# Performance work log

Measured on AMD Instinct MI355X. Metric: run time of the kernel, lower is better.

## Reference

```python
import jax, jax.numpy as jnp
from jax import lax
import numpy as np

B, M, LH, K, F, NA, NO = 16, 32, 128, 16, 3, 4, 1


def _conv(x, w, b):
    # x: (B,H,W,Cin), w: (kh,kw,Cin,Cout) -> (B,H,W,Cout), SAME zero padding
    return lax.conv_general_dilated(x, w, (1, 1), 'SAME',
                                    dimension_numbers=('NHWC', 'HWIO', 'NHWC')) + b


def setup_inputs() -> dict:
    key = jax.random.key(0)
    ks = jax.random.split(key, 14)
    s = 0.05
    inp = {
        'map_design': jax.random.uniform(ks[0], (B, NO, M, M), jnp.float32),
        'goal_map':   jax.random.uniform(ks[1], (B, 1, M, M), jnp.float32),
        'W_hid': jax.random.normal(ks[2], (3, 3, NO + 1, LH), jnp.float32) * s,
        'b_hid': jax.random.normal(ks[3], (LH,), jnp.float32) * s,
        'W_h0':  jax.random.normal(ks[4], (3, 3, LH, LH), jnp.float32) * s,
        'b_h0':  jax.random.normal(ks[5], (LH,), jnp.float32) * s,
        'W_c0':  jax.random.normal(ks[6], (3, 3, LH, LH), jnp.float32) * s,
        'b_c0':  jax.random.normal(ks[7], (LH,), jnp.float32) * s,
        'W_f':   jax.random.normal(ks[8], (F, F, LH, 1), jnp.float32) * s,
        'b_f':   jax.random.normal(ks[9], (1,), jnp.float32) * s,
        'W_ih':  jax.random.normal(ks[10], (4 * LH, 1), jnp.float32) * s,
        'b_ih':  jax.random.normal(ks[11], (4 * LH,), jnp.float32) * s,
        'W_hh':  jax.random.normal(ks[12], (4 * LH, LH), jnp.float32) * s,
        'b_hh':  jnp.zeros((4 * LH,), jnp.float32),
        'W_pol': jax.random.normal(ks[13], (LH, NA * NO), jnp.float32) * s,
    }
    return inp


def reference(map_design, goal_map, W_hid, b_hid, W_h0, b_h0, W_c0, b_c0,
              W_f, b_f, W_ih, b_ih, W_hh, b_hh, W_pol):
    # NCHW -> NHWC
    X = jnp.concatenate([map_design, goal_map], axis=1).transpose(0, 2, 3, 1)
    hid = _conv(X, W_hid, b_hid)                      # (B,M,M,LH)
    h0 = _conv(hid, W_h0, b_h0)                       # (B,M,M,LH)
    c0 = _conv(hid, W_c0, b_c0)

    def step(carry, _):
        h, c = carry                                  # (B,M,M,LH)
        inp = _conv(h, W_f, b_f).reshape(-1, 1)       # per-pixel scalar input
        hf = h.reshape(-1, LH)
        gates = inp @ W_ih.T + b_ih + hf @ W_hh.T + b_hh   # (BMM, 4*LH)
        i, f, g, o = jnp.split(gates, 4, axis=-1)     # torch LSTMCell order i,f,g,o
        i, f, o = jax.nn.sigmoid(i), jax.nn.sigmoid(f), jax.nn.sigmoid(o)
        g = jnp.tanh(g)
        c2 = f * c.reshape(-1, LH) + i * g
        h2 = o * jnp.tanh(c2)
        return (h2.reshape(B, M, M, LH), c2.reshape(B, M, M, LH)), None

    (hk, _), _ = lax.scan(step, (h0, c0), None, length=K - 1)

    # policy: 1x1 conv == per-pixel matmul
    logits_hw = jnp.einsum('bhwc,ca->bhwa', hk, W_pol)     # (B,M,M,NA*NO)
    logits = logits_hw.transpose(0, 3, 1, 2)               # (B,NA*NO,M,M)
    probs = jax.nn.softmax(logits.reshape(B * NO, NA, M, M), axis=1)
    logits = logits.reshape(B, NO, NA, M, M).transpose(0, 2, 1, 3, 4)
    probs = probs.reshape(B, NO, NA, M, M).transpose(0, 2, 1, 3, 4)
    return logits, probs
```

## Files before the change

kernel.cpp:

```cpp
#include <hip/hip_runtime.h>

#define MM 32
#define LH 128
#define NSTEPS 15
#define SSTR 136
#define NBLK 512
#define FSTR 32
#define SIDX(row,pxi,ch) (((row)*34 + (pxi))*SSTR + (ch))

typedef __bf16  bf16x8  __attribute__((ext_vector_type(8)));
typedef float   floatx4 __attribute__((ext_vector_type(4)));
typedef unsigned long long ull;

#define L2E 1.4426950408889634f

__device__ __forceinline__ float ex2(float x){
#if __has_builtin(__builtin_amdgcn_exp2f)
  return __builtin_amdgcn_exp2f(x);
#else
  float r; asm volatile("v_exp_f32 %0, %1\n\ts_nop 0" : "=v"(r) : "v"(x)); return r;
#endif
}
__device__ __forceinline__ float frcp(float x){ return __builtin_amdgcn_rcpf(x); }

__device__ __forceinline__ unsigned short cvt_bf16(float x){
  __bf16 b = (__bf16)x; unsigned short u; __builtin_memcpy(&u, &b, 2); return u;
}
__device__ __forceinline__ float bf2f(unsigned short u){
  union { unsigned u2; float f; } v; v.u2 = ((unsigned)u) << 16;
  return v.f;
}

__device__ __forceinline__ void st_dev(ull* p, ull v){
  __hip_atomic_store(p, v, __ATOMIC_RELAXED, __HIP_MEMORY_SCOPE_AGENT);
}
__device__ __forceinline__ ull ld_dev(ull* p){
  return __hip_atomic_load(p, __ATOMIC_RELAXED, __HIP_MEMORY_SCOPE_AGENT);
}
__device__ __forceinline__ void wait_flag(int* f, int target){
  while ((int)(__hip_atomic_load(f, __ATOMIC_RELAXED, __HIP_MEMORY_SCOPE_AGENT) - target) < 0){
    __builtin_amdgcn_s_sleep(1);
  }
}
__device__ __forceinline__ void set_flag(int* f, int v){
  __hip_atomic_store(f, v, __ATOMIC_RELAXED, __HIP_MEMORY_SCOPE_AGENT);
}

__global__ __launch_bounds__(512, 4) void k_mega(
    const float* __restrict__ mp,   const float* __restrict__ gl,
    const float* __restrict__ W_hid,const float* __restrict__ b_hid,
    const float* __restrict__ W_h0, const float* __restrict__ b_h0,
    const float* __restrict__ W_c0, const float* __restrict__ b_c0,
    const float* __restrict__ Wf,   const float* __restrict__ bfs,
    const float* __restrict__ wih,  const float* __restrict__ bih,
    const float* __restrict__ Whh,  const float* __restrict__ bhh,
    const float* __restrict__ wpol,
    unsigned short* __restrict__ wc0, unsigned short* __restrict__ wc1,
    unsigned short* __restrict__ whhf, float* __restrict__ bsum,
    unsigned short* __restrict__ wfbF,
    ull* __restrict__ expbuf,
    int* __restrict__ flags, float* __restrict__ out)
{
  __shared__ __attribute__((aligned(16))) unsigned short sH[3*34*SSTR];
  __shared__ float sCv[3][3][36];
  __shared__ float sOwn[32];
  __shared__ float sImp[2][32];

  int t = threadIdx.x, blk = blockIdx.x;
  int y = blk & 31, b = blk >> 5;
  int wave = t >> 6, l = t & 63, m16 = l & 15, quad = l >> 4;
  bool hasU = (y > 0), hasD = (y < 31);
  int ch = wave*16 + m16;

  for (int c = blk*512 + t; c < 91904; c += NBLK*512){
    if (c < 73728){
      int which = (c >= 36864) ? 1 : 0;
      int cc = which ? c - 36864 : c;
      int i2 = cc*4, frag = i2 >> 9, rem = i2 & 511, ll = rem >> 3, e0 = rem & 7;
      int kk = frag >> 5, ct = (frag >> 2) & 7, kc = frag & 3;
      int co = ct*16 + (ll & 15), ci0 = kc*32 + ((ll >> 4) << 3) + e0;
      const float* src = which ? W_c0 : W_h0;
      ull v = 0;
      #pragma unroll
      for (int j=0;j<4;j++) v |= (ull)cvt_bf16(src[(kk<<14) + (ci0+j)*128 + co]) << (16*j);
      st_dev((ull*)(which ? wc1 : wc0) + cc, v);
    } else if (c < 90112){
      int cc = c - 73728;
      int i2 = cc*4, frag = i2 >> 9, rem = i2 & 511, ll = rem >> 3, e0 = rem & 7;
      int q = frag >> 5, ct = (frag >> 2) & 7, kc = frag & 3;
      float scq = (q == 2) ? (2.f*L2E) : (-L2E);
      int rw = q*128 + ct*16 + (ll & 15), col = kc*32 + ((ll >> 4) << 3) + e0;
      const float* s4 = Whh + rw*128 + col;
      ull v = 0;
      #pragma unroll
      for (int j=0;j<4;j++) v |= (ull)cvt_bf16(s4[j]*scq) << (16*j);
      st_dev((ull*)whhf + cc, v);
    } else if (c < 90368){
      int cc = c - 90112; int j = cc*2;
      union { float f[2]; ull u; } pv;
      pv.f[0] = bih[j] + bhh[j]; pv.f[1] = bih[j+1] + bhh[j+1];
      st_dev((ull*)bsum + cc, pv.u);
    } else {
      int cc = c - 90368;
      int i2 = cc*4, frag = i2 >> 9, rem = i2 & 511, ll = rem >> 3, e0 = rem & 7;
      int ky = frag >> 2, kc = frag & 3;
      int n = ll & 15, k0 = kc*32 + ((ll >> 4) << 3) + e0;
      ull v = 0;
      if (n < 3){
        #pragma unroll
        for (int j=0;j<4;j++) v |= (ull)cvt_bf16(Wf[(ky*3 + n)*128 + k0 + j]) << (16*j);
      }
      st_dev((ull*)wfbF + cc, v);
    }
  }
  if (t < 128){
    int p = t >> 6, w2 = t & 63;
    st_dev(expbuf + ((size_t)p*NBLK + blk)*64 + w2, 0);
  }
  __syncthreads();
  if (t == 0) set_flag(&flags[blk*FSTR], 1);

  {
    int hch = t & 127, grp = t >> 7;
    float wz0[9], wz1[9];
    #pragma unroll
    for (int kk=0;kk<9;kk++){ wz0[kk] = W_hid[(kk*2)*LH + hch];
                              wz1[kk] = W_hid[(kk*2+1)*LH + hch]; }
    float bh = b_hid[hch];
    for (int i = 0; i < 24; i++){
      int rp = grp*24 + i, row = rp >> 5, x = rp & 31;
      int yi = y - 1 + row;
      float acc2 = 0.f;
      if (yi >= 0 && yi < MM){
        acc2 = bh;
        #pragma unroll
        for (int ky=0; ky<3; ky++){
          int yy = yi + ky - 1; if (yy < 0 || yy >= MM) continue;
          #pragma unroll
          for (int kx=0; kx<3; kx++){
            int xx = x + kx - 1; if (xx < 0 || xx >= MM) continue;
            int gi = (b*MM + yy)*MM + xx;
            acc2 += mp[gi]*wz0[ky*3+kx] + gl[gi]*wz1[ky*3+kx];
          }
        }
      }
      sH[SIDX(row, x+1, hch)] = cvt_bf16(acc2);
    }
  }
  if (t < 192){
    int k = t >> 6, col = ((t >> 5) & 1) ? 33 : 0, c4 = t & 31;
    *(ull*)&sH[SIDX(k, col, c4*4)] = 0;
  }
  if (t < 3){ sCv[t][0][32] = 0.f; sCv[t][2][1] = 0.f; }
  if (t < 180) wait_flag(&flags[t*FSTR], 1);
  __syncthreads();

  float c_reg[2][4];
  {
    floatx4 acch[2], accc[2];
    #pragma unroll
    for (int mt=0;mt<2;mt++){ acch[mt] = (floatx4){0.f,0.f,0.f,0.f};
                              accc[mt] = (floatx4){0.f,0.f,0.f,0.f}; }
    #pragma unroll
    for (int kk=0; kk<9; kk++){
      int ky = kk/3, kx = kk%3;
      #pragma unroll
      for (int kc=0; kc<4; kc++){
        int frag = ((kk*8 + wave)*4 + kc);
        bf16x8 b0 = *(const bf16x8*)(wc0 + (frag << 9) + l*8);
        bf16x8 b1 = *(const bf16x8*)(wc1 + (frag << 9) + l*8);
        #pragma unroll
        for (int mt=0; mt<2; mt++){
          bf16x8 a = *(const bf16x8*)&sH[SIDX(ky, m16 + mt*16 + kx, kc*32 + quad*8)];
          acch[mt] = __builtin_amdgcn_mfma_f32_16x16x32_bf16(a, b0, acch[mt], 0,0,0);
          accc[mt] = __builtin_amdgcn_mfma_f32_16x16x32_bf16(a, b1, accc[mt], 0,0,0);
        }
      }
    }
    __syncthreads();
    float bh = b_h0[ch], bc = b_c0[ch];
    #pragma unroll
    for (int mt=0; mt<2; mt++)
      #pragma unroll
      for (int r=0; r<4; r++){
        int px = mt*16 + quad*4 + r;
        c_reg[mt][r] = accc[mt][r] + bc;
        sH[SIDX(1, px+1, ch)] = cvt_bf16(acch[mt][r] + bh);
      }
  }
  __syncthreads();

  int cky = (wave == 0) ? 2 : ((wave == 1) ? 0 : 1);
  bf16x8 wfC[4];
  if (wave < 3){
    #pragma unroll
    for (int kc=0;kc<4;kc++)
      wfC[kc] = *(const bf16x8*)(wfbF + (((cky*4 + kc) << 9) + l*8));
  }
  float wv[4], bs[4];
  #pragma unroll
  for (int q=0;q<4;q++){
    float scq = (q == 2) ? (2.f*L2E) : (-L2E);
    int g = q*128 + ch;
    wv[q] = wih[g]*scq; bs[q] = bsum[g]*scq;
  }
  float bf0 = bfs[0];

  for (int s = 0; s < NSTEPS; s++){
    int cur = s & 1;

    bool doRole = (wave == 2) || (wave == 0 && hasU) || (wave == 1 && hasD);
    if (wave < 3 && doRole){
      floatx4 p0 = (floatx4){0.f,0.f,0.f,0.f};
      floatx4 p1 = (floatx4){0.f,0.f,0.f,0.f};
      #pragma unroll
      for (int kc=0;kc<4;kc++){
        bf16x8 aL = *(const bf16x8*)&sH[SIDX(1, m16 + 1,  kc*32 + quad*8)];
        bf16x8 aR = *(const bf16x8*)&sH[SIDX(1, m16 + 17, kc*32 + quad*8)];
        p0 = __builtin_amdgcn_mfma_f32_16x16x32_bf16(aL, wfC[kc], p0, 0,0,0);
        p1 = __builtin_amdgcn_mfma_f32_16x16x32_bf16(aR, wfC[kc], p1, 0,0,0);
      }
      if (m16 < 3){
        #pragma unroll
        for (int r=0;r<4;r++){
          sCv[wave][m16][quad*4 + r + m16]      = p0[r];
          sCv[wave][m16][16 + quad*4 + r + m16] = p1[r];
        }
      }
      __asm__ __volatile__("" ::: "memory");
      if (l < 32){
        float v = sCv[wave][0][l+1] + sCv[wave][1][l+1] + sCv[wave][2][l+1];
        if (wave == 2){
          sOwn[l] = bf0 + v;
        } else {
          union { float f; unsigned u; } pv; pv.f = v;
          st_dev(expbuf + ((size_t)cur*NBLK + blk)*64 + (wave == 1 ? 32 : 0) + l,
                 ((ull)(unsigned)(2 + s) << 32) | (ull)pv.u);
        }
      }
    }

    ull wa = (ull)whhf;
    asm volatile("" : "+v"(wa));
    const unsigned short* wp = (const unsigned short*)wa;
    floatx4 acc[2][4];
    #pragma unroll
    for (int mt=0;mt<2;mt++)
      #pragma unroll
      for (int q=0;q<4;q++) acc[mt][q] = (floatx4){0.f,0.f,0.f,0.f};
    #pragma unroll
    for (int kc=0; kc<4; kc++){
      bf16x8 a0 = *(const bf16x8*)&sH[SIDX(1, m16 + 1,  kc*32 + quad*8)];
      bf16x8 a1 = *(const bf16x8*)&sH[SIDX(1, m16 + 17, kc*32 + quad*8)];
      #pragma unroll
      for (int q=0; q<4; q++){
        bf16x8 bq = *(const bf16x8*)(wp + ((q*32 + wave*4 + kc) << 9) + l*8);
        acc[0][q] = __builtin_amdgcn_mfma_f32_16x16x32_bf16(a0, bq, acc[0][q], 0,0,0);
        acc[1][q] = __builtin_amdgcn_mfma_f32_16x16x32_bf16(a1, bq, acc[1][q], 0,0,0);
      }
    }

    if (wave == 3){
      int d = l >> 5, x = l & 31;
      bool ok = d ? hasD : hasU;
      float v = 0.f;
      if (ok){
        ull* p = expbuf + ((size_t)cur*NBLK + (d ? blk+1 : blk-1))*64 + (d ? 0 : 32) + x;
        ull vv;
        do { vv = ld_dev(p); } while ((int)((unsigned)(vv >> 32) - (unsigned)(2 + s)) < 0);
        union { unsigned u; float f; } pv; pv.u = (unsigned)vv; v = pv.f;
      }
      sImp[d][x] = v;
    }
    __syncthreads();

    #pragma unroll
    for (int mt=0; mt<2; mt++){
      #pragma unroll
      for (int r=0; r<4; r++){
        int px = mt*16 + quad*4 + r;
        float iv = sOwn[px] + sImp[0][px] + sImp[1][px];
        float p0 = acc[mt][0][r] + iv*wv[0] + bs[0];
        float p1 = acc[mt][1][r] + iv*wv[1] + bs[1];
        float p2 = acc[mt][2][r] + iv*wv[2] + bs[2];
        float p3 = acc[mt][3][r] + iv*wv[3] + bs[3];
        float ig = frcp(1.f + ex2(p0));
        float fg = frcp(1.f + ex2(p1));
        float gg = 1.f - 2.f*frcp(1.f + ex2(p2));
        float og = frcp(1.f + ex2(p3));
        float cn = fg*c_reg[mt][r] + ig*gg;
        c_reg[mt][r] = cn;
        float th = 1.f - 2.f*frcp(1.f + ex2((2.f*L2E)*cn));
        sH[SIDX(1, px+1, ch)] = cvt_bf16(og*th);
      }
    }
    __syncthreads();
  }

  {
    int px = t >> 4, s16 = t & 15;
    int base = SIDX(1, px+1, s16*8);
    uint4 h0v = *(const uint4*)&sH[base];
    float la[4] = {0.f,0.f,0.f,0.f};
    const unsigned short* hu = (const unsigned short*)&h0v;
    #pragma unroll
    for (int e=0;e<8;e++){
      int c = s16*8 + e; float hv2 = bf2f(hu[e]);
      const float* w4 = wpol + c*4;
      la[0]+=hv2*w4[0]; la[1]+=hv2*w4[1]; la[2]+=hv2*w4[2]; la[3]+=hv2*w4[3];
    }
    #pragma unroll
    for (int a=0;a<4;a++){
      la[a] += __shfl_xor(la[a], 1, 64);
      la[a] += __shfl_xor(la[a], 2, 64);
      la[a] += __shfl_xor(la[a], 4, 64);
      la[a] += __shfl_xor(la[a], 8, 64);
    }
    if (s16 == 0){
      float m = fmaxf(fmaxf(la[0],la[1]),fmaxf(la[2],la[3]));
      float e[4]; float sum = 0.f;
      #pragma unroll
      for (int a=0;a<4;a++){ e[a]=__expf(la[a]-m); sum+=e[a]; }
      float inv = frcp(sum);
      #pragma unroll
      for (int a=0;a<4;a++){
        int o = ((b*4 + a)*MM + y)*MM + px;
        out[o] = la[a];
        out[65536 + o] = e[a]*inv;
      }
    }
  }
}

extern "C" void kernel_launch(void* const* d_in, const int* in_sizes, int n_in,
                              void* d_out, int out_size, void* d_ws, size_t ws_size,
                              hipStream_t stream){
  const float* mp    = (const float*)d_in[0];
  const float* gl    = (const float*)d_in[1];
  const float* W_hid = (const float*)d_in[2];
  const float* b_hid = (const float*)d_in[3];
  const float* W_h0  = (const float*)d_in[4];
  const float* b_h0  = (const float*)d_in[5];
  const float* W_c0  = (const float*)d_in[6];
  const float* b_c0  = (const float*)d_in[7];
  const float* W_f   = (const float*)d_in[8];
  const float* b_f   = (const float*)d_in[9];
  const float* W_ih  = (const float*)d_in[10];
  const float* b_ih  = (const float*)d_in[11];
  const float* W_hh  = (const float*)d_in[12];
  const float* b_hh  = (const float*)d_in[13];
  const float* W_pol = (const float*)d_in[14];
  float* out = (float*)d_out;

  char* ws = (char*)d_ws;
  unsigned short* whhf  = (unsigned short*)ws;
  float*          bsum  = (float*)(ws + (128<<10));
  unsigned short* wc0   = (unsigned short*)(ws + (132<<10));
  unsigned short* wc1   = (unsigned short*)(ws + (420<<10));
  unsigned short* wfbF  = (unsigned short*)(ws + (708<<10));
  int*            flags = (int*)(ws + (720<<10));
  ull*            expbuf= (ull*)(ws + (784<<10));

  k_mega<<<NBLK, 512, 0, stream>>>(
      mp, gl, W_hid, b_hid, W_h0, b_h0, W_c0, b_c0, W_f, b_f,
      W_ih, b_ih, W_hh, b_hh, W_pol,
      wc0, wc1, whhf, bsum, wfbF, expbuf, flags, out);
}
```

Before: 181.8 us.

## Assign two image rows per block and keep recurrent weights in registers

Each persistent block now owns two adjacent rows instead of one, which halves the block count and the number of cross-block halo exchanges per LSTM step. The vertical filter convolution between the two owned rows is computed locally in six waves. The W_hh fragments are loaded once into registers instead of being re-read from global memory every step. In exchange each block does twice the work per step, uses more registers (launch bounds lowered to 2 blocks per CU), and the halo-polling loop is restructured with a prefetched load and raised priority on the exporting waves.

```diff
diff --git a/kernel.cpp b/kernel.cpp
--- a/kernel.cpp
+++ b/kernel.cpp
@@ -4,7 +4,7 @@
 #define LH 128
 #define NSTEPS 15
 #define SSTR 136
-#define NBLK 512
+#define NBLK 256
 #define FSTR 32
 #define SIDX(row,pxi,ch) (((row)*34 + (pxi))*SSTR + (ch))
 
@@ -46,7 +46,7 @@
   __hip_atomic_store(f, v, __ATOMIC_RELAXED, __HIP_MEMORY_SCOPE_AGENT);
 }
 
-__global__ __launch_bounds__(512, 4) void k_mega(
+__global__ __launch_bounds__(512, 2) void k_mega(
     const float* __restrict__ mp,   const float* __restrict__ gl,
     const float* __restrict__ W_hid,const float* __restrict__ b_hid,
     const float* __restrict__ W_h0, const float* __restrict__ b_h0,
@@ -61,15 +61,16 @@
     ull* __restrict__ expbuf,
     int* __restrict__ flags, float* __restrict__ out)
 {
-  __shared__ __attribute__((aligned(16))) unsigned short sH[3*34*SSTR];
-  __shared__ float sCv[3][3][36];
-  __shared__ float sOwn[32];
+  __shared__ __attribute__((aligned(16))) unsigned short sH[4*34*SSTR];
+  __shared__ float sCv[6][3][36];
+  __shared__ float sOwn[2][2][32];
   __shared__ float sImp[2][32];
 
   int t = threadIdx.x, blk = blockIdx.x;
-  int y = blk & 31, b = blk >> 5;
+  int pair = blk & 15, b = blk >> 4;
+  int y0 = pair*2;
   int wave = t >> 6, l = t & 63, m16 = l & 15, quad = l >> 4;
-  bool hasU = (y > 0), hasD = (y < 31);
+  bool hasU = (pair > 0), hasD = (pair < 15);
   int ch = wave*16 + m16;
 
   for (int c = blk*512 + t; c < 91904; c += NBLK*512){
@@ -121,17 +122,17 @@
   if (t == 0) set_flag(&flags[blk*FSTR], 1);
 
   {
-    int hch = t & 127, grp = t >> 7;
+    int hch = t & 127, g = t >> 7;
     float wz0[9], wz1[9];
     #pragma unroll
     for (int kk=0;kk<9;kk++){ wz0[kk] = W_hid[(kk*2)*LH + hch];
                               wz1[kk] = W_hid[(kk*2+1)*LH + hch]; }
     float bh = b_hid[hch];
-    for (int i = 0; i < 24; i++){
-      int rp = grp*24 + i, row = rp >> 5, x = rp & 31;
-      int yi = y - 1 + row;
+    int yi = y0 - 1 + g;
+    bool valid = (yi >= 0 && yi < MM);
+    for (int x = 0; x < MM; x++){
       float acc2 = 0.f;
-      if (yi >= 0 && yi < MM){
+      if (valid){
         acc2 = bh;
         #pragma unroll
         for (int ky=0; ky<3; ky++){
@@ -144,22 +145,22 @@
           }
         }
       }
-      sH[SIDX(row, x+1, hch)] = cvt_bf16(acc2);
-    }
-  }
-  if (t < 192){
+      sH[SIDX(g, x+1, hch)] = cvt_bf16(acc2);
+    }
+  }
+  if (t < 256){
     int k = t >> 6, col = ((t >> 5) & 1) ? 33 : 0, c4 = t & 31;
     *(ull*)&sH[SIDX(k, col, c4*4)] = 0;
   }
-  if (t < 3){ sCv[t][0][32] = 0.f; sCv[t][2][1] = 0.f; }
+  if (t < 6){ sCv[t][0][32] = 0.f; sCv[t][2][1] = 0.f; }
   if (t < 180) wait_flag(&flags[t*FSTR], 1);
   __syncthreads();
 
-  float c_reg[2][4];
+  float c_reg[4][4];
   {
-    floatx4 acch[2], accc[2];
-    #pragma unroll
-    for (int mt=0;mt<2;mt++){ acch[mt] = (floatx4){0.f,0.f,0.f,0.f};
+    floatx4 acch[4], accc[4];
+    #pragma unroll
+    for (int mt=0;mt<4;mt++){ acch[mt] = (floatx4){0.f,0.f,0.f,0.f};
                               accc[mt] = (floatx4){0.f,0.f,0.f,0.f}; }
     #pragma unroll
     for (int kk=0; kk<9; kk++){
@@ -170,8 +171,8 @@
         bf16x8 b0 = *(const bf16x8*)(wc0 + (frag << 9) + l*8);
         bf16x8 b1 = *(const bf16x8*)(wc1 + (frag << 9) + l*8);
         #pragma unroll
-        for (int mt=0; mt<2; mt++){
-          bf16x8 a = *(const bf16x8*)&sH[SIDX(ky, m16 + mt*16 + kx, kc*32 + quad*8)];
+        for (int mt=0; mt<4; mt++){
+          bf16x8 a = *(const bf16x8*)&sH[SIDX((mt>>1)+ky, m16 + (mt&1)*16 + kx, kc*32 + quad*8)];
           acch[mt] = __builtin_amdgcn_mfma_f32_16x16x32_bf16(a, b0, acch[mt], 0,0,0);
           accc[mt] = __builtin_amdgcn_mfma_f32_16x16x32_bf16(a, b1, accc[mt], 0,0,0);
         }
@@ -180,22 +181,29 @@
     __syncthreads();
     float bh = b_h0[ch], bc = b_c0[ch];
     #pragma unroll
-    for (int mt=0; mt<2; mt++)
+    for (int mt=0; mt<4; mt++)
       #pragma unroll
       for (int r=0; r<4; r++){
         int px = mt*16 + quad*4 + r;
         c_reg[mt][r] = accc[mt][r] + bc;
-        sH[SIDX(1, px+1, ch)] = cvt_bf16(acch[mt][r] + bh);
+        sH[SIDX(1+(px>>5), (px&31)+1, ch)] = cvt_bf16(acch[mt][r] + bh);
       }
   }
   __syncthreads();
 
-  int cky = (wave == 0) ? 2 : ((wave == 1) ? 0 : 1);
+  bf16x8 bfr[4][4];
+  #pragma unroll
+  for (int q=0;q<4;q++)
+    #pragma unroll
+    for (int kc=0;kc<4;kc++)
+      bfr[q][kc] = *(const bf16x8*)(whhf + (((q*32 + wave*4 + kc) << 9)) + l*8);
+
+  int ri = wave & 1, rky = wave >> 1;
   bf16x8 wfC[4];
-  if (wave < 3){
+  if (wave < 6){
     #pragma unroll
     for (int kc=0;kc<4;kc++)
-      wfC[kc] = *(const bf16x8*)(wfbF + (((cky*4 + kc) << 9) + l*8));
+      wfC[kc] = *(const bf16x8*)(wfbF + (((rky*4 + kc) << 9) + l*8));
   }
   float wv[4], bs[4];
   #pragma unroll
@@ -209,77 +217,92 @@
   for (int s = 0; s < NSTEPS; s++){
     int cur = s & 1;
 
-    bool doRole = (wave == 2) || (wave == 0 && hasU) || (wave == 1 && hasD);
-    if (wave < 3 && doRole){
-      floatx4 p0 = (floatx4){0.f,0.f,0.f,0.f};
-      floatx4 p1 = (floatx4){0.f,0.f,0.f,0.f};
-      #pragma unroll
-      for (int kc=0;kc<4;kc++){
-        bf16x8 aL = *(const bf16x8*)&sH[SIDX(1, m16 + 1,  kc*32 + quad*8)];
-        bf16x8 aR = *(const bf16x8*)&sH[SIDX(1, m16 + 17, kc*32 + quad*8)];
-        p0 = __builtin_amdgcn_mfma_f32_16x16x32_bf16(aL, wfC[kc], p0, 0,0,0);
-        p1 = __builtin_amdgcn_mfma_f32_16x16x32_bf16(aR, wfC[kc], p1, 0,0,0);
-      }
-      if (m16 < 3){
-        #pragma unroll
-        for (int r=0;r<4;r++){
-          sCv[wave][m16][quad*4 + r + m16]      = p0[r];
-          sCv[wave][m16][16 + quad*4 + r + m16] = p1[r];
-        }
-      }
-      __asm__ __volatile__("" ::: "memory");
-      if (l < 32){
-        float v = sCv[wave][0][l+1] + sCv[wave][1][l+1] + sCv[wave][2][l+1];
-        if (wave == 2){
-          sOwn[l] = bf0 + v;
-        } else {
-          union { float f; unsigned u; } pv; pv.f = v;
-          st_dev(expbuf + ((size_t)cur*NBLK + blk)*64 + (wave == 1 ? 32 : 0) + l,
-                 ((ull)(unsigned)(2 + s) << 32) | (ull)pv.u);
-        }
-      }
-    }
-
-    ull wa = (ull)whhf;
-    asm volatile("" : "+v"(wa));
-    const unsigned short* wp = (const unsigned short*)wa;
-    floatx4 acc[2][4];
-    #pragma unroll
-    for (int mt=0;mt<2;mt++)
+    if (wave < 6){
+      bool isExp = (wave == 1) || (wave == 4);
+      bool doit = !isExp || (wave == 1 ? hasD : hasU);
+      if (doit){
+        if (isExp) __builtin_amdgcn_s_setprio(1);
+        floatx4 p0 = (floatx4){0.f,0.f,0.f,0.f};
+        floatx4 p1 = (floatx4){0.f,0.f,0.f,0.f};
+        #pragma unroll
+        for (int kc=0;kc<4;kc++){
+          bf16x8 aL = *(const bf16x8*)&sH[SIDX(1+ri, m16 + 1,  kc*32 + quad*8)];
+          bf16x8 aR = *(const bf16x8*)&sH[SIDX(1+ri, m16 + 17, kc*32 + quad*8)];
+          p0 = __builtin_amdgcn_mfma_f32_16x16x32_bf16(aL, wfC[kc], p0, 0,0,0);
+          p1 = __builtin_amdgcn_mfma_f32_16x16x32_bf16(aR, wfC[kc], p1, 0,0,0);
+        }
+        if (m16 < 3){
+          #pragma unroll
+          for (int r=0;r<4;r++){
+            sCv[wave][m16][quad*4 + r + m16]      = p0[r];
+            sCv[wave][m16][16 + quad*4 + r + m16] = p1[r];
+          }
+        }
+        __asm__ __volatile__("" ::: "memory");
+        if (l < 32){
+          float v = sCv[wave][0][l+1] + sCv[wave][1][l+1] + sCv[wave][2][l+1];
+          if (wave == 1 || wave == 4){
+            union { float f; unsigned u; } pv; pv.f = v;
+            ull pk = ((ull)(unsigned)(2 + s) << 32) | (ull)pv.u;
+            st_dev(expbuf + ((size_t)cur*NBLK + blk)*64 + (wave == 1 ? 32 : 0) + l, pk);
+          } else if (wave == 0){
+            sOwn[1][0][l] = bf0 + v;
+          } else if (wave == 2){
+            sOwn[0][0][l] = bf0 + v;
+          } else if (wave == 3){
+            sOwn[1][1][l] = v;
+          } else {
+            sOwn[0][1][l] = v;
+          }
+        }
+        if (isExp) __builtin_amdgcn_s_setprio(0);
+      }
+    }
+
+    floatx4 acc[4][4];
+    #pragma unroll
+    for (int mt=0;mt<4;mt++)
       #pragma unroll
       for (int q=0;q<4;q++) acc[mt][q] = (floatx4){0.f,0.f,0.f,0.f};
     #pragma unroll
     for (int kc=0; kc<4; kc++){
-      bf16x8 a0 = *(const bf16x8*)&sH[SIDX(1, m16 + 1,  kc*32 + quad*8)];
-      bf16x8 a1 = *(const bf16x8*)&sH[SIDX(1, m16 + 17, kc*32 + quad*8)];
-      #pragma unroll
-      for (int q=0; q<4; q++){
-        bf16x8 bq = *(const bf16x8*)(wp + ((q*32 + wave*4 + kc) << 9) + l*8);
-        acc[0][q] = __builtin_amdgcn_mfma_f32_16x16x32_bf16(a0, bq, acc[0][q], 0,0,0);
-        acc[1][q] = __builtin_amdgcn_mfma_f32_16x16x32_bf16(a1, bq, acc[1][q], 0,0,0);
-      }
-    }
-
-    if (wave == 3){
+      bf16x8 a[4];
+      #pragma unroll
+      for (int mt=0;mt<4;mt++)
+        a[mt] = *(const bf16x8*)&sH[SIDX(1+(mt>>1), m16 + (mt&1)*16 + 1, kc*32 + quad*8)];
+      #pragma unroll
+      for (int q=0; q<4; q++)
+        #pragma unroll
+        for (int mt=0; mt<4; mt++)
+          acc[mt][q] = __builtin_amdgcn_mfma_f32_16x16x32_bf16(a[mt], bfr[q][kc], acc[mt][q], 0,0,0);
+    }
+
+    if (wave == 7){
       int d = l >> 5, x = l & 31;
       bool ok = d ? hasD : hasU;
       float v = 0.f;
       if (ok){
         ull* p = expbuf + ((size_t)cur*NBLK + (d ? blk+1 : blk-1))*64 + (d ? 0 : 32) + x;
-        ull vv;
-        do { vv = ld_dev(p); } while ((int)((unsigned)(vv >> 32) - (unsigned)(2 + s)) < 0);
-        union { unsigned u; float f; } pv; pv.u = (unsigned)vv; v = pv.f;
+        unsigned tgt = (unsigned)(2 + s);
+        ull c0 = ld_dev(p);
+        ull c1 = ld_dev(p);
+        while ((int)((unsigned)(c0 >> 32) - tgt) < 0){
+          c0 = c1;
+          c1 = ld_dev(p);
+        }
+        union { unsigned u; float f; } pv; pv.u = (unsigned)c0; v = pv.f;
       }
       sImp[d][x] = v;
     }
     __syncthreads();
 
     #pragma unroll
-    for (int mt=0; mt<2; mt++){
+    for (int mt=0; mt<4; mt++){
+      int row = mt >> 1;
       #pragma unroll
       for (int r=0; r<4; r++){
-        int px = mt*16 + quad*4 + r;
-        float iv = sOwn[px] + sImp[0][px] + sImp[1][px];
+        int x = ((mt & 1) << 4) + quad*4 + r;
+        float iv = sOwn[row][0][x] + sOwn[row][1][x] + sImp[row][x];
         float p0 = acc[mt][0][r] + iv*wv[0] + bs[0];
         float p1 = acc[mt][1][r] + iv*wv[1] + bs[1];
         float p2 = acc[mt][2][r] + iv*wv[2] + bs[2];
@@ -291,21 +314,29 @@
         float cn = fg*c_reg[mt][r] + ig*gg;
         c_reg[mt][r] = cn;
         float th = 1.f - 2.f*frcp(1.f + ex2((2.f*L2E)*cn));
-        sH[SIDX(1, px+1, ch)] = cvt_bf16(og*th);
+        sH[SIDX(1+row, x+1, ch)] = cvt_bf16(og*th);
       }
     }
     __syncthreads();
   }
 
   {
-    int px = t >> 4, s16 = t & 15;
-    int base = SIDX(1, px+1, s16*8);
+    int px = t >> 3, s8 = t & 7;
+    int base = SIDX(1+(px>>5), (px&31)+1, s8*16);
     uint4 h0v = *(const uint4*)&sH[base];
+    uint4 h1v = *(const uint4*)&sH[base + 8];
     float la[4] = {0.f,0.f,0.f,0.f};
     const unsigned short* hu = (const unsigned short*)&h0v;
     #pragma unroll
     for (int e=0;e<8;e++){
-      int c = s16*8 + e; float hv2 = bf2f(hu[e]);
+      int c = s8*16 + e; float hv2 = bf2f(hu[e]);
+      const float* w4 = wpol + c*4;
+      la[0]+=hv2*w4[0]; la[1]+=hv2*w4[1]; la[2]+=hv2*w4[2]; la[3]+=hv2*w4[3];
+    }
+    hu = (const unsigned short*)&h1v;
+    #pragma unroll
+    for (int e=0;e<8;e++){
+      int c = s8*16 + 8 + e; float hv2 = bf2f(hu[e]);
       const float* w4 = wpol + c*4;
       la[0]+=hv2*w4[0]; la[1]+=hv2*w4[1]; la[2]+=hv2*w4[2]; la[3]+=hv2*w4[3];
     }
@@ -314,9 +345,9 @@
       la[a] += __shfl_xor(la[a], 1, 64);
       la[a] += __shfl_xor(la[a], 2, 64);
       la[a] += __shfl_xor(la[a], 4, 64);
-      la[a] += __shfl_xor(la[a], 8, 64);
-    }
-    if (s16 == 0){
+    }
+    if (s8 == 0){
+      int y = y0 + (px>>5), x = px & 31;
       float m = fmaxf(fmaxf(la[0],la[1]),fmaxf(la[2],la[3]));
       float e[4]; float sum = 0.f;
       #pragma unroll
@@ -324,7 +355,7 @@
       float inv = frcp(sum);
       #pragma unroll
       for (int a=0;a<4;a++){
-        int o = ((b*4 + a)*MM + y)*MM + px;
+        int o = ((b*4 + a)*MM + y)*MM + x;
         out[o] = la[a];
         out[65536 + o] = e[a]*inv;
       }
```

After: 170.3 us. 6.3% less time.
